# Performance work log

Hardware: AMD Instinct MI355X
Metric: run time of the kernel (lower is better)

The kernel has to match this reference:

```python
import jax, jax.numpy as jnp
import numpy as np

N_POINTS = 2_000_000
GRID = (128, 128, 128)
N_COMP = 3


def _bspline_weights(u):
    # cubic B-spline basis, returns tuple of 4 arrays shaped like u
    u2 = u * u
    u3 = u2 * u
    w0 = (1.0 - u) ** 3 / 6.0
    w1 = (3.0 * u3 - 6.0 * u2 + 4.0) / 6.0
    w2 = (-3.0 * u3 + 3.0 * u2 + 3.0 * u + 1.0) / 6.0
    w3 = u3 / 6.0
    return (w0, w1, w2, w3)


def setup_inputs() -> dict:
    key = jax.random.key(0)
    kx, ky, kz, kp = jax.random.split(key, 4)
    # query points uniform in the supported domain [-1, 1]
    x = jax.random.uniform(kx, (N_POINTS,), jnp.float32, -1.0, 1.0)
    y = jax.random.uniform(ky, (N_POINTS,), jnp.float32, -1.0, 1.0)
    z = jax.random.uniform(kz, (N_POINTS,), jnp.float32, -1.0, 1.0)
    phi_x = jax.random.normal(kp, (*GRID, N_COMP), jnp.float32)
    return {"x": x, "y": y, "z": z, "phi_x": phi_x}


def reference(x, y, z, phi_x):
    # BSplineField3d.vectorized_displacement with support_outside=True,
    # default support_range=None -> spacing = 2/(n-3), origin = -1 - spacing.
    nx, ny, nz, _ = phi_x.shape
    dx = 2.0 / (nx - 3)
    dy = 2.0 / (ny - 3)
    dz = 2.0 / (nz - 3)
    ox, oy, oz = -1.0 - dx, -1.0 - dy, -1.0 - dz

    u = (x - ox - dx) / dx
    v = (y - oy - dy) / dy
    w = (z - oz - dz) / dz
    ix = jnp.floor(u).astype(jnp.int32)
    iy = jnp.floor(v).astype(jnp.int32)
    iz = jnp.floor(w).astype(jnp.int32)
    u = u - ix
    v = v - iy
    w = w - iz

    wu = _bspline_weights(u)
    wv = _bspline_weights(v)
    ww = _bspline_weights(w)

    T = jnp.zeros((x.shape[0], phi_x.shape[-1]), dtype=x.dtype)
    # 64 fixed taps: gather from control grid at clamped indices, MAC.
    for l in range(4):
        ixl = jnp.clip(ix + l, 0, nx - 1)
        for m in range(4):
            iym = jnp.clip(iy + m, 0, ny - 1)
            wum = wu[l] * wv[m]
            for n in range(4):
                izn = jnp.clip(iz + n, 0, nz - 1)
                coef = wum * ww[n]  # [N]
                T = T + coef[:, None] * phi_x[ixl, iym, izn]  # gather [N, C]
    return T
```

## Files before the change

### kernel.cpp

```cpp
#include <hip/hip_runtime.h>


#define NBINS 4096
#define NBLK  256
#define W4STRIDE 25

__device__ __forceinline__ void bspline_w(float u, float& w0, float& w1,
                                          float& w2, float& w3) {
    const float u2 = u * u;
    const float u3 = u2 * u;
    const float t  = 1.0f - u;
    w0 = t * t * t * (1.0f / 6.0f);
    w1 = (3.0f * u3 - 6.0f * u2 + 4.0f) * (1.0f / 6.0f);
    w2 = (-3.0f * u3 + 3.0f * u2 + 3.0f * u + 1.0f) * (1.0f / 6.0f);
    w3 = u3 * (1.0f / 6.0f);
}

__device__ __forceinline__ int point_bin(float x, float y, float z) {
    const float dx = 2.0f / 125.0f;
    const float ox = -1.0f - dx;
    const int ix = (int)floorf((x - ox - dx) / dx);
    const int iy = (int)floorf((y - ox - dx) / dx);
    const int iz = (int)floorf((z - ox - dx) / dx);
    const int bx = min(max(ix, 0), 127) >> 3;
    const int by = min(max(iy, 0), 127) >> 3;
    const int bz = min(max(iz, 0), 127) >> 3;
    return (bx << 8) | (by << 4) | bz;
}

__global__ __launch_bounds__(1024) void hist_kernel(
    const float* __restrict__ xs, const float* __restrict__ ys,
    const float* __restrict__ zs, unsigned* __restrict__ hist,
    int n, int chunk) {
    __shared__ unsigned h[NBINS];
    for (int j = threadIdx.x; j < NBINS; j += 1024) h[j] = 0;
    __syncthreads();
    const int b = blockIdx.x;
    const int lo = b * chunk;
    const int hi = min(n, lo + chunk);
    for (int base = lo + threadIdx.x * 4; base < hi; base += 1024 * 4) {
        if (base + 4 <= hi) {
            const float4 x4 = *reinterpret_cast<const float4*>(xs + base);
            const float4 y4 = *reinterpret_cast<const float4*>(ys + base);
            const float4 z4 = *reinterpret_cast<const float4*>(zs + base);
            atomicAdd(&h[point_bin(x4.x, y4.x, z4.x)], 1u);
            atomicAdd(&h[point_bin(x4.y, y4.y, z4.y)], 1u);
            atomicAdd(&h[point_bin(x4.z, y4.z, z4.z)], 1u);
            atomicAdd(&h[point_bin(x4.w, y4.w, z4.w)], 1u);
        } else {
            for (int i = base; i < hi; ++i)
                atomicAdd(&h[point_bin(xs[i], ys[i], zs[i])], 1u);
        }
    }
    __syncthreads();
    for (int j = threadIdx.x; j < NBINS; j += 1024) hist[b * NBINS + j] = h[j];
}

__global__ __launch_bounds__(256) void colscan_kernel(
    unsigned* __restrict__ hist, unsigned* __restrict__ total) {
    const int j = blockIdx.x * 256 + threadIdx.x;
    unsigned run = 0;
#pragma unroll 16
    for (int b = 0; b < NBLK; ++b) {
        const unsigned c = hist[b * NBINS + j];
        hist[b * NBINS + j] = run;
        run += c;
    }
    total[j] = run;
}

__global__ __launch_bounds__(1024) void scan_kernel(
    const unsigned* __restrict__ total, unsigned* __restrict__ binbase) {
    __shared__ unsigned sdata[1024];
    const int t = threadIdx.x;
    const unsigned v0 = total[4 * t + 0];
    const unsigned v1 = total[4 * t + 1];
    const unsigned v2 = total[4 * t + 2];
    const unsigned v3 = total[4 * t + 3];
    sdata[t] = v0 + v1 + v2 + v3;
    __syncthreads();
    for (int off = 1; off < 1024; off <<= 1) {
        unsigned x = (t >= off) ? sdata[t - off] : 0u;
        __syncthreads();
        sdata[t] += x;
        __syncthreads();
    }
    const unsigned ex = (t > 0) ? sdata[t - 1] : 0u;
    binbase[4 * t + 0] = ex;
    binbase[4 * t + 1] = ex + v0;
    binbase[4 * t + 2] = ex + v0 + v1;
    binbase[4 * t + 3] = ex + v0 + v1 + v2;
}

__global__ __launch_bounds__(1024) void scatter_kernel(
    const float* __restrict__ xs, const float* __restrict__ ys,
    const float* __restrict__ zs, const unsigned* __restrict__ hist,
    const unsigned* __restrict__ binbase, float4* __restrict__ rec,
    int n, int chunk) {
    __shared__ unsigned off[NBINS];
    const int b = blockIdx.x;
    for (int j = threadIdx.x; j < NBINS; j += 1024)
        off[j] = hist[b * NBINS + j] + binbase[j];
    __syncthreads();
    const int lo = b * chunk;
    const int hi = min(n, lo + chunk);
    for (int base = lo + threadIdx.x * 4; base < hi; base += 1024 * 4) {
        if (base + 4 <= hi) {
            const float4 x4 = *reinterpret_cast<const float4*>(xs + base);
            const float4 y4 = *reinterpret_cast<const float4*>(ys + base);
            const float4 z4 = *reinterpret_cast<const float4*>(zs + base);
            unsigned p;
            p = atomicAdd(&off[point_bin(x4.x, y4.x, z4.x)], 1u);
            rec[p] = make_float4(x4.x, y4.x, z4.x, __int_as_float(base + 0));
            p = atomicAdd(&off[point_bin(x4.y, y4.y, z4.y)], 1u);
            rec[p] = make_float4(x4.y, y4.y, z4.y, __int_as_float(base + 1));
            p = atomicAdd(&off[point_bin(x4.z, y4.z, z4.z)], 1u);
            rec[p] = make_float4(x4.z, y4.z, z4.z, __int_as_float(base + 2));
            p = atomicAdd(&off[point_bin(x4.w, y4.w, z4.w)], 1u);
            rec[p] = make_float4(x4.w, y4.w, z4.w, __int_as_float(base + 3));
        } else {
            for (int i = base; i < hi; ++i) {
                const float x = xs[i], y = ys[i], z = zs[i];
                const unsigned p = atomicAdd(&off[point_bin(x, y, z)], 1u);
                rec[p] = make_float4(x, y, z, __int_as_float(i));
            }
        }
    }
}

__global__ __launch_bounds__(512, 6) void eval_kernel(
    const float4* __restrict__ rec, const unsigned* __restrict__ binbase,
    const unsigned* __restrict__ total, const float* __restrict__ phi,
    float* __restrict__ out) {
    const int bin = blockIdx.x;
    const unsigned cnt = total[bin];
    if (cnt == 0) return;
    const unsigned start = binbase[bin];

    const int gx0 = ((bin >> 8) & 15) << 3;
    const int gy0 = ((bin >> 4) & 15) << 3;
    const int gz0 = (bin & 15) << 3;

    __shared__ float raw[31 * 36];
    __shared__ float4 W4[121 * W4STRIDE];

    for (int r0 = 0; r0 < 121; r0 += 31) {
        const int nr = min(31, 121 - r0);
        if (gz0 <= 112) {
            for (int p = threadIdx.x; p < nr * 9; p += 512) {
                const int rr = p / 9, q = p - rr * 9;
                const int row = r0 + rr;
                const int lx = row / 11, ly = row - lx * 11;
                const int gx = min(gx0 + lx, 127);
                const int gy = min(gy0 + ly, 127);
                const float* src =
                    phi + (size_t)((gx * 128 + gy) * 128 + gz0) * 3 + q * 4;
                *reinterpret_cast<float4*>(&raw[rr * 36 + q * 4]) =
                    *reinterpret_cast<const float4*>(src);
            }
        } else {
            for (int p = threadIdx.x; p < nr * 11; p += 512) {
                const int rr = p / 11, zz = p - rr * 11;
                const int row = r0 + rr;
                const int lx = row / 11, ly = row - lx * 11;
                const int gx = min(gx0 + lx, 127);
                const int gy = min(gy0 + ly, 127);
                const int z  = min(gz0 + zz, 127);
                const float* s = phi + (size_t)((gx * 128 + gy) * 128 + z) * 3;
                raw[rr * 36 + zz * 3 + 0] = s[0];
                raw[rr * 36 + zz * 3 + 1] = s[1];
                raw[rr * 36 + zz * 3 + 2] = s[2];
            }
        }
        __syncthreads();
        for (int p = threadIdx.x; p < nr * 24; p += 512) {
            const int rr = p / 24, t = p - rr * 24;
            const int s = t / 3, c = t - 3 * s;
            const float* r = &raw[rr * 36 + s * 3 + c];
            W4[(r0 + rr) * W4STRIDE + t] = make_float4(r[0], r[3], r[6], r[9]);
        }
        __syncthreads();
    }

    const float dx = 2.0f / 125.0f;
    const float ox = -1.0f - dx;

    for (unsigned k = start + threadIdx.x; k < start + cnt; k += 512) {
        const float4 r4 = rec[k];
        const int idx = __float_as_int(r4.w);

        const float U = (r4.x - ox - dx) / dx;
        const float V = (r4.y - ox - dx) / dx;
        const float Z = (r4.z - ox - dx) / dx;
        const float fu = floorf(U), fv = floorf(V), fw = floorf(Z);
        const int ix = (int)fu, iy = (int)fv, iz = (int)fw;
        const float u = U - fu, v = V - fv, w = Z - fw;

        float wu[4], wv[4], wz[4];
        bspline_w(u, wu[0], wu[1], wu[2], wu[3]);
        bspline_w(v, wv[0], wv[1], wv[2], wv[3]);
        bspline_w(w, wz[0], wz[1], wz[2], wz[3]);

        int izb = iz < 0 ? 0 : iz;
        const bool sh = izb > 124;
        if (sh) izb = 124;
        const float zw0 = sh ? 0.0f : wz[0];
        const float zw1 = sh ? wz[0] : wz[1];
        const float zw2 = sh ? wz[1] : wz[2];
        const float zw3 = sh ? (wz[2] + wz[3]) : wz[3];
        const int lzb3 = (izb - gz0) * 3;

        int lxi[4], lyi[4];
#pragma unroll
        for (int l = 0; l < 4; ++l) {
            lxi[l] = min(max(ix + l, 0), 127) - gx0;
            lyi[l] = min(max(iy + l, 0), 127) - gy0;
        }

        float acc0 = 0.0f, acc1 = 0.0f, acc2 = 0.0f;
#pragma unroll
        for (int l = 0; l < 4; ++l) {
            const int rowx = lxi[l] * 11;
#pragma unroll
            for (int m = 0; m < 4; ++m) {
                const int base = (rowx + lyi[m]) * W4STRIDE + lzb3;
                const float4 a  = W4[base + 0];
                const float4 bb = W4[base + 1];
                const float4 cc = W4[base + 2];
                const float wm = wu[l] * wv[m];
                const float c0 = wm * zw0;
                const float c1 = wm * zw1;
                const float c2 = wm * zw2;
                const float c3 = wm * zw3;
                acc0 = fmaf(c0, a.x, acc0);
                acc0 = fmaf(c1, a.y, acc0);
                acc0 = fmaf(c2, a.z, acc0);
                acc0 = fmaf(c3, a.w, acc0);
                acc1 = fmaf(c0, bb.x, acc1);
                acc1 = fmaf(c1, bb.y, acc1);
                acc1 = fmaf(c2, bb.z, acc1);
                acc1 = fmaf(c3, bb.w, acc1);
                acc2 = fmaf(c0, cc.x, acc2);
                acc2 = fmaf(c1, cc.y, acc2);
                acc2 = fmaf(c2, cc.z, acc2);
                acc2 = fmaf(c3, cc.w, acc2);
            }
        }
        float* o = out + 3 * (size_t)idx;
        o[0] = acc0;
        o[1] = acc1;
        o[2] = acc2;
    }
}

__global__ __launch_bounds__(256) void bspline3d_direct(
    const float* __restrict__ xs, const float* __restrict__ ys,
    const float* __restrict__ zs, const float* __restrict__ phi,
    float* __restrict__ out, int n) {
    const int i = blockIdx.x * blockDim.x + threadIdx.x;
    if (i >= n) return;
    const float dx = 2.0f / 125.0f;
    const float ox = -1.0f - dx;
    float u = (xs[i] - ox - dx) / dx;
    float v = (ys[i] - ox - dx) / dx;
    float w = (zs[i] - ox - dx) / dx;
    const float fu = floorf(u), fv = floorf(v), fw = floorf(w);
    const int ix = (int)fu, iy = (int)fv, iz = (int)fw;
    u -= fu; v -= fv; w -= fw;
    float wu[4], wv[4], wz[4];
    bspline_w(u, wu[0], wu[1], wu[2], wu[3]);
    bspline_w(v, wv[0], wv[1], wv[2], wv[3]);
    bspline_w(w, wz[0], wz[1], wz[2], wz[3]);
    int izb = iz < 0 ? 0 : iz;
    const bool sh = izb > 124;
    if (sh) izb = 124;
    const float zw0 = sh ? 0.0f : wz[0];
    const float zw1 = sh ? wz[0] : wz[1];
    const float zw2 = sh ? wz[1] : wz[2];
    const float zw3 = sh ? (wz[2] + wz[3]) : wz[3];
    int xi[4], yi[4];
#pragma unroll
    for (int l = 0; l < 4; ++l) {
        xi[l] = min(max(ix + l, 0), 127);
        yi[l] = min(max(iy + l, 0), 127);
    }
    const float* pz = phi + izb * 3;
    float acc0 = 0.0f, acc1 = 0.0f, acc2 = 0.0f;
#pragma unroll
    for (int l = 0; l < 4; ++l) {
        const int rowx = xi[l] << 7;
#pragma unroll
        for (int m = 0; m < 4; ++m) {
            const float* p = pz + (rowx + yi[m]) * 384;
            const float4 a = *reinterpret_cast<const float4*>(p);
            const float4 b = *reinterpret_cast<const float4*>(p + 4);
            const float4 c = *reinterpret_cast<const float4*>(p + 8);
            const float wm = wu[l] * wv[m];
            const float c0 = wm * zw0, c1 = wm * zw1, c2 = wm * zw2, c3 = wm * zw3;
            acc0 = fmaf(c0, a.x, acc0); acc1 = fmaf(c0, a.y, acc1); acc2 = fmaf(c0, a.z, acc2);
            acc0 = fmaf(c1, a.w, acc0); acc1 = fmaf(c1, b.x, acc1); acc2 = fmaf(c1, b.y, acc2);
            acc0 = fmaf(c2, b.z, acc0); acc1 = fmaf(c2, b.w, acc1); acc2 = fmaf(c2, c.x, acc2);
            acc0 = fmaf(c3, c.y, acc0); acc1 = fmaf(c3, c.z, acc1); acc2 = fmaf(c3, c.w, acc2);
        }
    }
    float* o = out + 3 * (size_t)i;
    o[0] = acc0; o[1] = acc1; o[2] = acc2;
}

extern "C" void kernel_launch(void* const* d_in, const int* in_sizes, int n_in,
                              void* d_out, int out_size, void* d_ws,
                              size_t ws_size, hipStream_t stream) {
    const float* xs  = (const float*)d_in[0];
    const float* ys  = (const float*)d_in[1];
    const float* zs  = (const float*)d_in[2];
    const float* phi = (const float*)d_in[3];
    float* out = (float*)d_out;
    const int n = in_sizes[0];

    const size_t hist_off  = 0;
    const size_t total_off = hist_off + (size_t)NBLK * NBINS * 4;
    const size_t base_off  = total_off + NBINS * 4;
    const size_t rec_off   = base_off + NBINS * 4;
    const size_t need = rec_off + (size_t)n * 16;

    if (ws_size < need) {
        bspline3d_direct<<<(n + 255) / 256, 256, 0, stream>>>(xs, ys, zs, phi,
                                                              out, n);
        return;
    }

    unsigned* hist    = (unsigned*)((char*)d_ws + hist_off);
    unsigned* total   = (unsigned*)((char*)d_ws + total_off);
    unsigned* binbase = (unsigned*)((char*)d_ws + base_off);
    float4*   rec     = (float4*)((char*)d_ws + rec_off);

    const int chunk = (((n + NBLK - 1) / NBLK) + 3) & ~3;

    hist_kernel<<<NBLK, 1024, 0, stream>>>(xs, ys, zs, hist, n, chunk);
    colscan_kernel<<<NBINS / 256, 256, 0, stream>>>(hist, total);
    scan_kernel<<<1, 1024, 0, stream>>>(total, binbase);
    scatter_kernel<<<NBLK, 1024, 0, stream>>>(xs, ys, zs, hist, binbase, rec,
                                              n, chunk);
    eval_kernel<<<NBINS, 512, 0, stream>>>(rec, binbase, total, phi, out);
}
```

Before: 194.3 us.

## Use packed FMA, multiply-by-reciprocal, 16-bit histograms and more binning blocks

```diff
diff --git a/kernel.cpp b/kernel.cpp
--- a/kernel.cpp
+++ b/kernel.cpp
@@ -2,8 +2,10 @@
 
 
 #define NBINS 4096
-#define NBLK  256
+#define NBLK  512
 #define W4STRIDE 25
+
+typedef float v2f __attribute__((ext_vector_type(2)));
 
 __device__ __forceinline__ void bspline_w(float u, float& w0, float& w1,
                                           float& w2, float& w3) {
@@ -17,11 +19,9 @@
 }
 
 __device__ __forceinline__ int point_bin(float x, float y, float z) {
-    const float dx = 2.0f / 125.0f;
-    const float ox = -1.0f - dx;
-    const int ix = (int)floorf((x - ox - dx) / dx);
-    const int iy = (int)floorf((y - ox - dx) / dx);
-    const int iz = (int)floorf((z - ox - dx) / dx);
+    const int ix = (int)floorf((x + 1.0f) * 62.5f);
+    const int iy = (int)floorf((y + 1.0f) * 62.5f);
+    const int iz = (int)floorf((z + 1.0f) * 62.5f);
     const int bx = min(max(ix, 0), 127) >> 3;
     const int by = min(max(iy, 0), 127) >> 3;
     const int bz = min(max(iz, 0), 127) >> 3;
@@ -30,7 +30,7 @@
 
 __global__ __launch_bounds__(1024) void hist_kernel(
     const float* __restrict__ xs, const float* __restrict__ ys,
-    const float* __restrict__ zs, unsigned* __restrict__ hist,
+    const float* __restrict__ zs, unsigned short* __restrict__ hist,
     int n, int chunk) {
     __shared__ unsigned h[NBINS];
     for (int j = threadIdx.x; j < NBINS; j += 1024) h[j] = 0;
@@ -53,17 +53,18 @@
         }
     }
     __syncthreads();
-    for (int j = threadIdx.x; j < NBINS; j += 1024) hist[b * NBINS + j] = h[j];
+    for (int j = threadIdx.x; j < NBINS; j += 1024)
+        hist[b * NBINS + j] = (unsigned short)h[j];
 }
 
 __global__ __launch_bounds__(256) void colscan_kernel(
-    unsigned* __restrict__ hist, unsigned* __restrict__ total) {
+    unsigned short* __restrict__ hist, unsigned* __restrict__ total) {
     const int j = blockIdx.x * 256 + threadIdx.x;
     unsigned run = 0;
 #pragma unroll 16
     for (int b = 0; b < NBLK; ++b) {
         const unsigned c = hist[b * NBINS + j];
-        hist[b * NBINS + j] = run;
+        hist[b * NBINS + j] = (unsigned short)run;
         run += c;
     }
     total[j] = run;
@@ -94,13 +95,13 @@
 
 __global__ __launch_bounds__(1024) void scatter_kernel(
     const float* __restrict__ xs, const float* __restrict__ ys,
-    const float* __restrict__ zs, const unsigned* __restrict__ hist,
+    const float* __restrict__ zs, const unsigned short* __restrict__ hist,
     const unsigned* __restrict__ binbase, float4* __restrict__ rec,
     int n, int chunk) {
     __shared__ unsigned off[NBINS];
     const int b = blockIdx.x;
     for (int j = threadIdx.x; j < NBINS; j += 1024)
-        off[j] = hist[b * NBINS + j] + binbase[j];
+        off[j] = (unsigned)hist[b * NBINS + j] + binbase[j];
     __syncthreads();
     const int lo = b * chunk;
     const int hi = min(n, lo + chunk);
@@ -182,16 +183,13 @@
         __syncthreads();
     }
 
-    const float dx = 2.0f / 125.0f;
-    const float ox = -1.0f - dx;
-
     for (unsigned k = start + threadIdx.x; k < start + cnt; k += 512) {
         const float4 r4 = rec[k];
         const int idx = __float_as_int(r4.w);
 
-        const float U = (r4.x - ox - dx) / dx;
-        const float V = (r4.y - ox - dx) / dx;
-        const float Z = (r4.z - ox - dx) / dx;
+        const float U = (r4.x + 1.0f) * 62.5f;
+        const float V = (r4.y + 1.0f) * 62.5f;
+        const float Z = (r4.z + 1.0f) * 62.5f;
         const float fu = floorf(U), fv = floorf(V), fw = floorf(Z);
         const int ix = (int)fu, iy = (int)fv, iz = (int)fw;
         const float u = U - fu, v = V - fv, w = Z - fw;
@@ -204,10 +202,11 @@
         int izb = iz < 0 ? 0 : iz;
         const bool sh = izb > 124;
         if (sh) izb = 124;
-        const float zw0 = sh ? 0.0f : wz[0];
-        const float zw1 = sh ? wz[0] : wz[1];
-        const float zw2 = sh ? wz[1] : wz[2];
-        const float zw3 = sh ? (wz[2] + wz[3]) : wz[3];
+        v2f zwLo, zwHi;
+        zwLo.x = sh ? 0.0f : wz[0];
+        zwLo.y = sh ? wz[0] : wz[1];
+        zwHi.x = sh ? wz[1] : wz[2];
+        zwHi.y = sh ? (wz[2] + wz[3]) : wz[3];
         const int lzb3 = (izb - gz0) * 3;
 
         int lxi[4], lyi[4];
@@ -217,7 +216,7 @@
             lyi[l] = min(max(iy + l, 0), 127) - gy0;
         }
 
-        float acc0 = 0.0f, acc1 = 0.0f, acc2 = 0.0f;
+        v2f acc0 = {0.0f, 0.0f}, acc1 = {0.0f, 0.0f}, acc2 = {0.0f, 0.0f};
 #pragma unroll
         for (int l = 0; l < 4; ++l) {
             const int rowx = lxi[l] * 11;
@@ -228,28 +227,23 @@
                 const float4 bb = W4[base + 1];
                 const float4 cc = W4[base + 2];
                 const float wm = wu[l] * wv[m];
-                const float c0 = wm * zw0;
-                const float c1 = wm * zw1;
-                const float c2 = wm * zw2;
-                const float c3 = wm * zw3;
-                acc0 = fmaf(c0, a.x, acc0);
-                acc0 = fmaf(c1, a.y, acc0);
-                acc0 = fmaf(c2, a.z, acc0);
-                acc0 = fmaf(c3, a.w, acc0);
-                acc1 = fmaf(c0, bb.x, acc1);
-                acc1 = fmaf(c1, bb.y, acc1);
-                acc1 = fmaf(c2, bb.z, acc1);
-                acc1 = fmaf(c3, bb.w, acc1);
-                acc2 = fmaf(c0, cc.x, acc2);
-                acc2 = fmaf(c1, cc.y, acc2);
-                acc2 = fmaf(c2, cc.z, acc2);
-                acc2 = fmaf(c3, cc.w, acc2);
+                const v2f cLo = wm * zwLo;
+                const v2f cHi = wm * zwHi;
+                v2f aLo = {a.x, a.y},  aHi = {a.z, a.w};
+                v2f bLo = {bb.x, bb.y}, bHi = {bb.z, bb.w};
+                v2f gLo = {cc.x, cc.y}, gHi = {cc.z, cc.w};
+                acc0 = __builtin_elementwise_fma(cLo, aLo, acc0);
+                acc0 = __builtin_elementwise_fma(cHi, aHi, acc0);
+                acc1 = __builtin_elementwise_fma(cLo, bLo, acc1);
+                acc1 = __builtin_elementwise_fma(cHi, bHi, acc1);
+                acc2 = __builtin_elementwise_fma(cLo, gLo, acc2);
+                acc2 = __builtin_elementwise_fma(cHi, gHi, acc2);
             }
         }
         float* o = out + 3 * (size_t)idx;
-        o[0] = acc0;
-        o[1] = acc1;
-        o[2] = acc2;
+        o[0] = acc0.x + acc0.y;
+        o[1] = acc1.x + acc1.y;
+        o[2] = acc2.x + acc2.y;
     }
 }
 
@@ -259,11 +253,9 @@
     float* __restrict__ out, int n) {
     const int i = blockIdx.x * blockDim.x + threadIdx.x;
     if (i >= n) return;
-    const float dx = 2.0f / 125.0f;
-    const float ox = -1.0f - dx;
-    float u = (xs[i] - ox - dx) / dx;
-    float v = (ys[i] - ox - dx) / dx;
-    float w = (zs[i] - ox - dx) / dx;
+    float u = (xs[i] + 1.0f) * 62.5f;
+    float v = (ys[i] + 1.0f) * 62.5f;
+    float w = (zs[i] + 1.0f) * 62.5f;
     const float fu = floorf(u), fv = floorf(v), fw = floorf(w);
     const int ix = (int)fu, iy = (int)fv, iz = (int)fw;
     u -= fu; v -= fv; w -= fw;
@@ -318,7 +310,7 @@
     const int n = in_sizes[0];
 
     const size_t hist_off  = 0;
-    const size_t total_off = hist_off + (size_t)NBLK * NBINS * 4;
+    const size_t total_off = hist_off + (size_t)NBLK * NBINS * 2;
     const size_t base_off  = total_off + NBINS * 4;
     const size_t rec_off   = base_off + NBINS * 4;
     const size_t need = rec_off + (size_t)n * 16;
@@ -329,10 +321,10 @@
         return;
     }
 
-    unsigned* hist    = (unsigned*)((char*)d_ws + hist_off);
-    unsigned* total   = (unsigned*)((char*)d_ws + total_off);
-    unsigned* binbase = (unsigned*)((char*)d_ws + base_off);
-    float4*   rec     = (float4*)((char*)d_ws + rec_off);
+    unsigned short* hist = (unsigned short*)((char*)d_ws + hist_off);
+    unsigned* total      = (unsigned*)((char*)d_ws + total_off);
+    unsigned* binbase    = (unsigned*)((char*)d_ws + base_off);
+    float4*   rec        = (float4*)((char*)d_ws + rec_off);
 
     const int chunk = (((n + NBLK - 1) / NBLK) + 3) & ~3;
 
```

After: 218.8 us. +12.6%, slower.
